# Kernel optimization log

Measured on AMD Instinct MI355X. Metric: run time of the kernel, lower is better.

Reference implementation:

```python
import jax, jax.numpy as jnp
import numpy as np

H = 4096      # hidden_size
HQ = 32       # num_attention_heads
HKV = 8       # num_key_value_heads
D = 128       # head_dim
I = 14336     # intermediate_size
T = 2048      # number of tokens (prefill)
THETA = 500000.0
EPS = 1e-5


def setup_inputs() -> dict:
    key = jax.random.key(0)
    ks = jax.random.split(key, 9)
    s = 0.02
    return {
        "hidden_states": jax.random.normal(ks[0], (T, H), jnp.float32),
        "position_ids": jnp.arange(T, dtype=jnp.int32),
        "w_q": jax.random.normal(ks[1], (H, H), jnp.float32) * s,
        "w_k": jax.random.normal(ks[2], (HKV * D, H), jnp.float32) * s,
        "w_v": jax.random.normal(ks[3], (HKV * D, H), jnp.float32) * s,
        "w_o": jax.random.normal(ks[4], (H, H), jnp.float32) * s,
        "w_gate": jax.random.normal(ks[5], (I, H), jnp.float32) * s,
        "w_up": jax.random.normal(ks[6], (I, H), jnp.float32) * s,
        "w_down": jax.random.normal(ks[7], (H, I), jnp.float32) * s,
        "rms1_w": jnp.ones((H,), jnp.float32),
        "rms2_w": jnp.ones((H,), jnp.float32),
    }


def _rmsnorm(x, w, eps=EPS):
    var = jnp.mean(jnp.square(x), axis=-1, keepdims=True)
    return x * jax.lax.rsqrt(var + eps) * w


def _rope(x, pos):
    # x: [T, n_heads, D], non-interleaved (rotate halves)
    inv_freq = 1.0 / (THETA ** (jnp.arange(0, D, 2, dtype=jnp.float32) / D))  # [D/2]
    freqs = pos.astype(jnp.float32)[:, None] * inv_freq[None, :]              # [T, D/2]
    cos = jnp.cos(freqs)[:, None, :]  # [T, 1, D/2]
    sin = jnp.sin(freqs)[:, None, :]
    x1, x2 = x[..., : D // 2], x[..., D // 2:]
    return jnp.concatenate([x1 * cos - x2 * sin, x2 * cos + x1 * sin], axis=-1)


def reference(hidden_states, position_ids, w_q, w_k, w_v, w_o,
              w_gate, w_up, w_down, rms1_w, rms2_w):
    x = hidden_states  # [T, H]
    # ---- attention block ----
    h = _rmsnorm(x, rms1_w)
    q = (h @ w_q.T).reshape(T, HQ, D)
    k = (h @ w_k.T).reshape(T, HKV, D)
    v = (h @ w_v.T).reshape(T, HKV, D)
    q = _rope(q, position_ids)
    k = _rope(k, position_ids)
    # GQA: expand kv heads to query heads
    group = HQ // HKV
    k = jnp.repeat(k, group, axis=1)  # [T, HQ, D]
    v = jnp.repeat(v, group, axis=1)
    scale = 1.0 / jnp.sqrt(jnp.float32(D))
    scores = jnp.einsum("qhd,khd->hqk", q, k) * scale  # [HQ, T, T]
    causal = jnp.tril(jnp.ones((T, T), dtype=bool))
    scores = jnp.where(causal[None, :, :], scores, jnp.finfo(scores.dtype).min)
    probs = jax.nn.softmax(scores, axis=-1)
    attn = jnp.einsum("hqk,khd->qhd", probs, v).reshape(T, H)
    x = x + attn @ w_o.T
    # ---- MLP block (SwiGLU) ----
    h = _rmsnorm(x, rms2_w)
    gate = jax.nn.silu(h @ w_gate.T)
    up = h @ w_up.T
    x = x + (gate * up) @ w_down.T
    return x
```

## Files before the change

kernel.cpp:

```cpp
#include <hip/hip_runtime.h>
#include <hip/hip_bf16.h>

#define T_ 2048
#define H_ 4096
#define HQ_ 32
#define HKV_ 8
#define D_ 128
#define I_ 14336

typedef __attribute__((ext_vector_type(8))) short bf16x8;
typedef __attribute__((ext_vector_type(4))) float f32x4;

__device__ __forceinline__ float bf2f(short s) {
    return __uint_as_float(((unsigned int)(unsigned short)s) << 16);
}
__device__ __forceinline__ short f2bf(float f) {
    __hip_bfloat16 h = __float2bfloat16(f);
    unsigned short u;
    __builtin_memcpy(&u, &h, 2);
    return (short)u;
}

__global__ __launch_bounds__(256) void rmsnorm_kernel(
    const float* __restrict__ x, const float* __restrict__ w,
    __hip_bfloat16* __restrict__ out)
{
    int t = blockIdx.x, tid = threadIdx.x;
    const float4* xp = (const float4*)(x + (size_t)t * H_);
    float4 v[4];
    float ss = 0.f;
#pragma unroll
    for (int i = 0; i < 4; ++i) {
        v[i] = xp[i * 256 + tid];
        ss += v[i].x * v[i].x + v[i].y * v[i].y + v[i].z * v[i].z + v[i].w * v[i].w;
    }
#pragma unroll
    for (int off = 32; off; off >>= 1) ss += __shfl_xor(ss, off, 64);
    __shared__ float red[4];
    int wave = tid >> 6, lane = tid & 63;
    if (lane == 0) red[wave] = ss;
    __syncthreads();
    float scale = rsqrtf((red[0] + red[1] + red[2] + red[3]) * (1.0f / H_) + 1e-5f);
    const float4* wp = (const float4*)w;
    uint2* op = (uint2*)(out + (size_t)t * H_);
#pragma unroll
    for (int i = 0; i < 4; ++i) {
        float4 wv = wp[i * 256 + tid];
        union { unsigned short u[4]; uint2 d; } o;
        o.u[0] = (unsigned short)f2bf(v[i].x * scale * wv.x);
        o.u[1] = (unsigned short)f2bf(v[i].y * scale * wv.y);
        o.u[2] = (unsigned short)f2bf(v[i].z * scale * wv.z);
        o.u[3] = (unsigned short)f2bf(v[i].w * scale * wv.w);
        op[i * 256 + tid] = o.d;
    }
}

template <int RESADD>
__global__ __launch_bounds__(256) void gemm_kernel(
    const __hip_bfloat16* __restrict__ A, const float* __restrict__ B,
    void* __restrict__ Cout, const float* __restrict__ res,
    int M, int N, int K)
{
    constexpr int BM = 128, BN = 128, BK = 32, LDA = 40;
    __shared__ __align__(16) __hip_bfloat16 As[BM * LDA];
    __shared__ __align__(16) __hip_bfloat16 Bs[BN * LDA];
    int tid = threadIdx.x;
    int wave = tid >> 6, lane = tid & 63, ln = lane & 15, quad = lane >> 4;
    int wr = wave >> 1, wc = wave & 1;
    int m0 = blockIdx.x * BM, n0 = blockIdx.y * BN;
    int srow = tid >> 1, shalf = tid & 1;

    f32x4 acc[4][4] = {};

    const uint4*  ag = (const uint4*)(A + (size_t)(m0 + srow) * K + shalf * 16);
    const float4* bg = (const float4*)(B + (size_t)(n0 + srow) * K + shalf * 16);

    for (int k0 = 0; k0 < K; k0 += BK) {
        uint4 a0 = ag[0], a1 = ag[1];
        ag += 4;
        float4 b0 = bg[0], b1 = bg[1], b2 = bg[2], b3 = bg[3];
        bg += 8;
        __syncthreads();
        *(uint4*)&As[srow * LDA + shalf * 16]     = a0;
        *(uint4*)&As[srow * LDA + shalf * 16 + 8] = a1;
        union { uint4 q[2]; unsigned short u[16]; } bb;
        float bf[16] = { b0.x, b0.y, b0.z, b0.w, b1.x, b1.y, b1.z, b1.w,
                         b2.x, b2.y, b2.z, b2.w, b3.x, b3.y, b3.z, b3.w };
#pragma unroll
        for (int j = 0; j < 16; ++j) bb.u[j] = (unsigned short)f2bf(bf[j]);
        *(uint4*)&Bs[srow * LDA + shalf * 16]     = bb.q[0];
        *(uint4*)&Bs[srow * LDA + shalf * 16 + 8] = bb.q[1];
        __syncthreads();

        bf16x8 af[4], bfr[4];
#pragma unroll
        for (int i = 0; i < 4; ++i)
            af[i] = *(const bf16x8*)&As[(wr * 64 + i * 16 + ln) * LDA + quad * 8];
#pragma unroll
        for (int j = 0; j < 4; ++j)
            bfr[j] = *(const bf16x8*)&Bs[(wc * 64 + j * 16 + ln) * LDA + quad * 8];
#pragma unroll
        for (int i = 0; i < 4; ++i)
#pragma unroll
            for (int j = 0; j < 4; ++j)
                acc[i][j] = __builtin_amdgcn_mfma_f32_16x16x32_bf16(af[i], bfr[j], acc[i][j], 0, 0, 0);
    }

#pragma unroll
    for (int i = 0; i < 4; ++i)
#pragma unroll
        for (int j = 0; j < 4; ++j)
#pragma unroll
            for (int r = 0; r < 4; ++r) {
                int row = m0 + wr * 64 + i * 16 + quad * 4 + r;
                int col = n0 + wc * 64 + j * 16 + ln;
                if (RESADD) {
                    ((float*)Cout)[(size_t)row * N + col] =
                        acc[i][j][r] + res[(size_t)row * N + col];
                } else {
                    ((__hip_bfloat16*)Cout)[(size_t)row * N + col] =
                        __float2bfloat16(acc[i][j][r]);
                }
            }
}

__global__ __launch_bounds__(64) void rope_kernel(
    __hip_bfloat16* __restrict__ q, __hip_bfloat16* __restrict__ k,
    const int* __restrict__ pos)
{
    int t = blockIdx.x, h = blockIdx.y, i = threadIdx.x;
    float p = (float)pos[t];
    float inv = powf(500000.0f, -(float)i * (1.0f / 64.0f));
    float s, c;
    sincosf(p * inv, &s, &c);
    __hip_bfloat16* base = (h < HQ_) ? (q + ((size_t)t * HQ_ + h) * D_)
                                     : (k + ((size_t)t * HKV_ + (h - HQ_)) * D_);
    float x1 = bf2f(*(short*)&base[i]);
    float x2 = bf2f(*(short*)&base[i + 64]);
    base[i]      = __float2bfloat16(x1 * c - x2 * s);
    base[i + 64] = __float2bfloat16(x2 * c + x1 * s);
}

__global__ __launch_bounds__(256) void attn_kernel(
    const __hip_bfloat16* __restrict__ Q,
    const __hip_bfloat16* __restrict__ K,
    const __hip_bfloat16* __restrict__ V,
    __hip_bfloat16* __restrict__ O)
{
    constexpr float scale = 0.08838834764831845f;
    int qtile = blockIdx.x, hq = blockIdx.y, hkv = hq >> 2;
    int tid = threadIdx.x;
    int wave = tid >> 6, lane = tid & 63, ln = lane & 15, quad = lane >> 4;
    int q0 = qtile * 64;

    __shared__ __align__(16) __hip_bfloat16 Kt[32 * 136];
    __shared__ __align__(16) __hip_bfloat16 Vt[128 * 40];
    __shared__ __align__(16) __hip_bfloat16 Pb[4][16 * 40];

    bf16x8 qf[4];
    {
        const __hip_bfloat16* qp = Q + ((size_t)(q0 + wave * 16 + ln) * HQ_ + hq) * D_;
#pragma unroll
        for (int kc = 0; kc < 4; ++kc)
            qf[kc] = *(const bf16x8*)(qp + kc * 32 + quad * 8);
    }

    f32x4 o_acc[8] = {};
    float m_run[4] = { -3e38f, -3e38f, -3e38f, -3e38f };
    float l_run[4] = { 0.f, 0.f, 0.f, 0.f };

    int nkt = (q0 + 64) / 32;
    int sr = tid >> 3, sseg = tid & 7;
    for (int kt = 0; kt < nkt; ++kt) {
        int k0 = kt * 32;
        {
            const __hip_bfloat16* kp = K + ((size_t)(k0 + sr) * HKV_ + hkv) * D_ + sseg * 16;
            uint4 k01 = ((const uint4*)kp)[0], k23 = ((const uint4*)kp)[1];
            *(uint4*)&Kt[sr * 136 + sseg * 16]     = k01;
            *(uint4*)&Kt[sr * 136 + sseg * 16 + 8] = k23;
            const __hip_bfloat16* vp = V + ((size_t)(k0 + sr) * HKV_ + hkv) * D_ + sseg * 16;
            union { uint4 q[2]; __hip_bfloat16 h[16]; } vv;
            vv.q[0] = ((const uint4*)vp)[0];
            vv.q[1] = ((const uint4*)vp)[1];
#pragma unroll
            for (int i = 0; i < 16; ++i) Vt[(sseg * 16 + i) * 40 + sr] = vv.h[i];
        }
        __syncthreads();

        f32x4 s_acc[2] = {};
#pragma unroll
        for (int ct = 0; ct < 2; ++ct)
#pragma unroll
            for (int kc = 0; kc < 4; ++kc) {
                bf16x8 kf = *(const bf16x8*)&Kt[(ct * 16 + ln) * 136 + kc * 32 + quad * 8];
                s_acc[ct] = __builtin_amdgcn_mfma_f32_16x16x32_bf16(qf[kc], kf, s_acc[ct], 0, 0, 0);
            }

        float pv[2][4], tmax[4];
#pragma unroll
        for (int r = 0; r < 4; ++r) {
            int qr = q0 + wave * 16 + quad * 4 + r;
            float s0 = s_acc[0][r] * scale;
            float s1 = s_acc[1][r] * scale;
            if (k0 + ln > qr) s0 = -1e30f;
            if (k0 + 16 + ln > qr) s1 = -1e30f;
            pv[0][r] = s0; pv[1][r] = s1;
            tmax[r] = fmaxf(s0, s1);
        }
#pragma unroll
        for (int off = 1; off < 16; off <<= 1)
#pragma unroll
            for (int r = 0; r < 4; ++r)
                tmax[r] = fmaxf(tmax[r], __shfl_xor(tmax[r], off, 64));

        float alpha[4], tsum[4];
#pragma unroll
        for (int r = 0; r < 4; ++r) {
            float mn = fmaxf(m_run[r], tmax[r]);
            alpha[r] = __expf(m_run[r] - mn);
            m_run[r] = mn;
            float p0 = __expf(pv[0][r] - mn);
            float p1 = __expf(pv[1][r] - mn);
            pv[0][r] = p0; pv[1][r] = p1;
            tsum[r] = p0 + p1;
        }
#pragma unroll
        for (int off = 1; off < 16; off <<= 1)
#pragma unroll
            for (int r = 0; r < 4; ++r)
                tsum[r] += __shfl_xor(tsum[r], off, 64);
#pragma unroll
        for (int r = 0; r < 4; ++r) l_run[r] = l_run[r] * alpha[r] + tsum[r];
#pragma unroll
        for (int nt = 0; nt < 8; ++nt)
#pragma unroll
            for (int r = 0; r < 4; ++r) o_acc[nt][r] *= alpha[r];

#pragma unroll
        for (int r = 0; r < 4; ++r) {
            Pb[wave][(quad * 4 + r) * 40 + ln]      = __float2bfloat16(pv[0][r]);
            Pb[wave][(quad * 4 + r) * 40 + 16 + ln] = __float2bfloat16(pv[1][r]);
        }
        asm volatile("s_waitcnt lgkmcnt(0)" ::: "memory");

        bf16x8 pf = *(const bf16x8*)&Pb[wave][ln * 40 + quad * 8];
#pragma unroll
        for (int nt = 0; nt < 8; ++nt) {
            bf16x8 vf = *(const bf16x8*)&Vt[(nt * 16 + ln) * 40 + quad * 8];
            o_acc[nt] = __builtin_amdgcn_mfma_f32_16x16x32_bf16(pf, vf, o_acc[nt], 0, 0, 0);
        }
        __syncthreads();
    }

    float inv_l[4];
#pragma unroll
    for (int r = 0; r < 4; ++r) inv_l[r] = 1.0f / l_run[r];
#pragma unroll
    for (int nt = 0; nt < 8; ++nt)
#pragma unroll
        for (int r = 0; r < 4; ++r) {
            int qr = q0 + wave * 16 + quad * 4 + r;
            O[(size_t)qr * H_ + hq * D_ + nt * 16 + ln] =
                __float2bfloat16(o_acc[nt][r] * inv_l[r]);
        }
}

__global__ __launch_bounds__(256) void silu_mul_kernel(
    __hip_bfloat16* __restrict__ gate, const __hip_bfloat16* __restrict__ up)
{
    size_t idx = (size_t)blockIdx.x * 256 + threadIdx.x;
    bf16x8 g = ((const bf16x8*)gate)[idx];
    bf16x8 u = ((const bf16x8*)up)[idx];
    bf16x8 o;
#pragma unroll
    for (int j = 0; j < 8; ++j) {
        float gf = bf2f(g[j]);
        float uf = bf2f(u[j]);
        float r = gf / (1.0f + __expf(-gf)) * uf;
        o[j] = f2bf(r);
    }
    ((bf16x8*)gate)[idx] = o;
}

extern "C" void kernel_launch(void* const* d_in, const int* in_sizes, int n_in,
                              void* d_out, int out_size, void* d_ws, size_t ws_size,
                              hipStream_t stream) {
    const float* x_in   = (const float*)d_in[0];
    const int*   pos    = (const int*)d_in[1];
    const float* w_q    = (const float*)d_in[2];
    const float* w_k    = (const float*)d_in[3];
    const float* w_v    = (const float*)d_in[4];
    const float* w_o    = (const float*)d_in[5];
    const float* w_gate = (const float*)d_in[6];
    const float* w_up   = (const float*)d_in[7];
    const float* w_down = (const float*)d_in[8];
    const float* rms1   = (const float*)d_in[9];
    const float* rms2   = (const float*)d_in[10];
    float* out = (float*)d_out;

    char* ws = (char*)d_ws;
    size_t off = 0;
    auto alloc = [&](size_t bytes) {
        void* p = ws + off;
        off += (bytes + 255) & ~(size_t)255;
        return p;
    };
    __hip_bfloat16* hb   = (__hip_bfloat16*)alloc((size_t)T_ * H_ * 2);
    __hip_bfloat16* qb   = (__hip_bfloat16*)alloc((size_t)T_ * HQ_ * D_ * 2);
    __hip_bfloat16* kb   = (__hip_bfloat16*)alloc((size_t)T_ * HKV_ * D_ * 2);
    __hip_bfloat16* vb   = (__hip_bfloat16*)alloc((size_t)T_ * HKV_ * D_ * 2);
    float*          x1   = (float*)alloc((size_t)T_ * H_ * 4);
    __hip_bfloat16* gate = (__hip_bfloat16*)alloc((size_t)T_ * I_ * 2);
    __hip_bfloat16* up   = (__hip_bfloat16*)alloc((size_t)T_ * I_ * 2);

    rmsnorm_kernel<<<T_, 256, 0, stream>>>(x_in, rms1, hb);
    gemm_kernel<0><<<dim3(16, 32), 256, 0, stream>>>(hb, w_q, qb, nullptr, T_, H_, H_);
    gemm_kernel<0><<<dim3(16, 8), 256, 0, stream>>>(hb, w_k, kb, nullptr, T_, HKV_ * D_, H_);
    gemm_kernel<0><<<dim3(16, 8), 256, 0, stream>>>(hb, w_v, vb, nullptr, T_, HKV_ * D_, H_);
    rope_kernel<<<dim3(T_, HQ_ + HKV_), 64, 0, stream>>>(qb, kb, pos);
    attn_kernel<<<dim3(32, 32), 256, 0, stream>>>(qb, kb, vb, hb);
    gemm_kernel<1><<<dim3(16, 32), 256, 0, stream>>>(hb, w_o, x1, x_in, T_, H_, H_);
    rmsnorm_kernel<<<T_, 256, 0, stream>>>(x1, rms2, qb);
    gemm_kernel<0><<<dim3(16, 112), 256, 0, stream>>>(qb, w_gate, gate, nullptr, T_, I_, H_);
    gemm_kernel<0><<<dim3(16, 112), 256, 0, stream>>>(qb, w_up, up, nullptr, T_, I_, H_);
    silu_mul_kernel<<<(T_ * I_ / 8) / 256, 256, 0, stream>>>(gate, up);
    gemm_kernel<1><<<dim3(16, 32), 256, 0, stream>>>(gate, w_down, out, x1, T_, H_, I_);
}
```

Measured before the change: 2.996 ms.

## Pre-convert weights to bf16 and stage GEMM tiles via direct global-to-LDS loads

Adds a pass that converts every fp32 weight matrix to bf16 in workspace on each call. The GEMM then reads bf16 weights through global_load_lds 16-byte direct-to-LDS copies instead of loading fp32, converting in registers and storing to padded LDS. Workgroup IDs are also remapped so consecutive tiles land on the same XCD for better L2 reuse. Costs include an extra read and write of all weights per call and unpadded LDS rows, which may cause bank conflicts on the fragment reads.

```diff
diff --git a/kernel.cpp b/kernel.cpp
--- a/kernel.cpp
+++ b/kernel.cpp
@@ -19,6 +19,30 @@
     unsigned short u;
     __builtin_memcpy(&u, &h, 2);
     return (short)u;
+}
+
+__device__ __forceinline__ void gload_lds16(const void* g, void* l) {
+    __builtin_amdgcn_global_load_lds(
+        (const __attribute__((address_space(1))) void*)g,
+        (__attribute__((address_space(3))) void*)l, 16, 0, 0);
+}
+
+__global__ __launch_bounds__(256) void w2bf_kernel(
+    const float* __restrict__ src, __hip_bfloat16* __restrict__ dst)
+{
+    size_t idx = ((size_t)blockIdx.x * 256 + threadIdx.x) * 8;
+    float4 a = *(const float4*)(src + idx);
+    float4 b = *(const float4*)(src + idx + 4);
+    union { unsigned short u[8]; uint4 q; } o;
+    o.u[0] = (unsigned short)f2bf(a.x);
+    o.u[1] = (unsigned short)f2bf(a.y);
+    o.u[2] = (unsigned short)f2bf(a.z);
+    o.u[3] = (unsigned short)f2bf(a.w);
+    o.u[4] = (unsigned short)f2bf(b.x);
+    o.u[5] = (unsigned short)f2bf(b.y);
+    o.u[6] = (unsigned short)f2bf(b.z);
+    o.u[7] = (unsigned short)f2bf(b.w);
+    *(uint4*)(dst + idx) = o.q;
 }
 
 __global__ __launch_bounds__(256) void rmsnorm_kernel(
@@ -57,48 +81,53 @@
 
 template <int RESADD>
 __global__ __launch_bounds__(256) void gemm_kernel(
-    const __hip_bfloat16* __restrict__ A, const float* __restrict__ B,
+    const __hip_bfloat16* __restrict__ A, const __hip_bfloat16* __restrict__ B,
     void* __restrict__ Cout, const float* __restrict__ res,
     int M, int N, int K)
 {
-    constexpr int BM = 128, BN = 128, BK = 32, LDA = 40;
-    __shared__ __align__(16) __hip_bfloat16 As[BM * LDA];
-    __shared__ __align__(16) __hip_bfloat16 Bs[BN * LDA];
+    constexpr int BM = 128, BN = 128, BK = 32;
+    __shared__ __align__(16) __hip_bfloat16 As[BM * BK];
+    __shared__ __align__(16) __hip_bfloat16 Bs[BN * BK];
     int tid = threadIdx.x;
     int wave = tid >> 6, lane = tid & 63, ln = lane & 15, quad = lane >> 4;
     int wr = wave >> 1, wc = wave & 1;
-    int m0 = blockIdx.x * BM, n0 = blockIdx.y * BN;
-    int srow = tid >> 1, shalf = tid & 1;
+
+    int nwg = gridDim.x * gridDim.y;
+    int orig = blockIdx.y * gridDim.x + blockIdx.x;
+    int xcd = orig & 7, loc = orig >> 3;
+    int qq = nwg >> 3, rr = nwg & 7;
+    int swz = (xcd < rr ? xcd * (qq + 1) : rr * (qq + 1) + (xcd - rr) * qq) + loc;
+    int m0 = (swz % gridDim.x) * BM;
+    int n0 = (swz / gridDim.x) * BN;
+
+    int row = tid >> 2, slot = tid & 3;
+    const __hip_bfloat16* ga0 = A + (size_t)(m0 + row) * K + slot * 8;
+    const __hip_bfloat16* ga1 = A + (size_t)(m0 + 64 + row) * K + slot * 8;
+    const __hip_bfloat16* gb0 = B + (size_t)(n0 + row) * K + slot * 8;
+    const __hip_bfloat16* gb1 = B + (size_t)(n0 + 64 + row) * K + slot * 8;
+    __hip_bfloat16* la0 = As + tid * 8;
+    __hip_bfloat16* la1 = As + 2048 + tid * 8;
+    __hip_bfloat16* lb0 = Bs + tid * 8;
+    __hip_bfloat16* lb1 = Bs + 2048 + tid * 8;
 
     f32x4 acc[4][4] = {};
 
-    const uint4*  ag = (const uint4*)(A + (size_t)(m0 + srow) * K + shalf * 16);
-    const float4* bg = (const float4*)(B + (size_t)(n0 + srow) * K + shalf * 16);
-
     for (int k0 = 0; k0 < K; k0 += BK) {
-        uint4 a0 = ag[0], a1 = ag[1];
-        ag += 4;
-        float4 b0 = bg[0], b1 = bg[1], b2 = bg[2], b3 = bg[3];
-        bg += 8;
         __syncthreads();
-        *(uint4*)&As[srow * LDA + shalf * 16]     = a0;
-        *(uint4*)&As[srow * LDA + shalf * 16 + 8] = a1;
-        union { uint4 q[2]; unsigned short u[16]; } bb;
-        float bf[16] = { b0.x, b0.y, b0.z, b0.w, b1.x, b1.y, b1.z, b1.w,
-                         b2.x, b2.y, b2.z, b2.w, b3.x, b3.y, b3.z, b3.w };
-#pragma unroll
-        for (int j = 0; j < 16; ++j) bb.u[j] = (unsigned short)f2bf(bf[j]);
-        *(uint4*)&Bs[srow * LDA + shalf * 16]     = bb.q[0];
-        *(uint4*)&Bs[srow * LDA + shalf * 16 + 8] = bb.q[1];
+        gload_lds16(ga0, la0);
+        gload_lds16(ga1, la1);
+        gload_lds16(gb0, lb0);
+        gload_lds16(gb1, lb1);
+        ga0 += BK; ga1 += BK; gb0 += BK; gb1 += BK;
         __syncthreads();
 
         bf16x8 af[4], bfr[4];
 #pragma unroll
         for (int i = 0; i < 4; ++i)
-            af[i] = *(const bf16x8*)&As[(wr * 64 + i * 16 + ln) * LDA + quad * 8];
+            af[i] = *(const bf16x8*)&As[(wr * 64 + i * 16 + ln) * BK + quad * 8];
 #pragma unroll
         for (int j = 0; j < 4; ++j)
-            bfr[j] = *(const bf16x8*)&Bs[(wc * 64 + j * 16 + ln) * LDA + quad * 8];
+            bfr[j] = *(const bf16x8*)&Bs[(wc * 64 + j * 16 + ln) * BK + quad * 8];
 #pragma unroll
         for (int i = 0; i < 4; ++i)
 #pragma unroll
@@ -112,13 +141,13 @@
         for (int j = 0; j < 4; ++j)
 #pragma unroll
             for (int r = 0; r < 4; ++r) {
-                int row = m0 + wr * 64 + i * 16 + quad * 4 + r;
-                int col = n0 + wc * 64 + j * 16 + ln;
+                int row_ = m0 + wr * 64 + i * 16 + quad * 4 + r;
+                int col_ = n0 + wc * 64 + j * 16 + ln;
                 if (RESADD) {
-                    ((float*)Cout)[(size_t)row * N + col] =
-                        acc[i][j][r] + res[(size_t)row * N + col];
+                    ((float*)Cout)[(size_t)row_ * N + col_] =
+                        acc[i][j][r] + res[(size_t)row_ * N + col_];
                 } else {
-                    ((__hip_bfloat16*)Cout)[(size_t)row * N + col] =
+                    ((__hip_bfloat16*)Cout)[(size_t)row_ * N + col_] =
                         __float2bfloat16(acc[i][j][r]);
                 }
             }
@@ -312,17 +341,35 @@
     float*          x1   = (float*)alloc((size_t)T_ * H_ * 4);
     __hip_bfloat16* gate = (__hip_bfloat16*)alloc((size_t)T_ * I_ * 2);
     __hip_bfloat16* up   = (__hip_bfloat16*)alloc((size_t)T_ * I_ * 2);
+    __hip_bfloat16* wqb  = (__hip_bfloat16*)alloc((size_t)H_ * H_ * 2);
+    __hip_bfloat16* wkb  = (__hip_bfloat16*)alloc((size_t)HKV_ * D_ * H_ * 2);
+    __hip_bfloat16* wvb  = (__hip_bfloat16*)alloc((size_t)HKV_ * D_ * H_ * 2);
+    __hip_bfloat16* wob  = (__hip_bfloat16*)alloc((size_t)H_ * H_ * 2);
+    __hip_bfloat16* wgb  = (__hip_bfloat16*)alloc((size_t)I_ * H_ * 2);
+    __hip_bfloat16* wub  = (__hip_bfloat16*)alloc((size_t)I_ * H_ * 2);
+    __hip_bfloat16* wdb  = (__hip_bfloat16*)alloc((size_t)H_ * I_ * 2);
+
+    auto cvt = [&](const float* s, __hip_bfloat16* d, size_t n) {
+        w2bf_kernel<<<(unsigned)(n / 2048), 256, 0, stream>>>(s, d);
+    };
+    cvt(w_q,    wqb, (size_t)H_ * H_);
+    cvt(w_k,    wkb, (size_t)HKV_ * D_ * H_);
+    cvt(w_v,    wvb, (size_t)HKV_ * D_ * H_);
+    cvt(w_o,    wob, (size_t)H_ * H_);
+    cvt(w_gate, wgb, (size_t)I_ * H_);
+    cvt(w_up,   wub, (size_t)I_ * H_);
+    cvt(w_down, wdb, (size_t)H_ * I_);
 
     rmsnorm_kernel<<<T_, 256, 0, stream>>>(x_in, rms1, hb);
-    gemm_kernel<0><<<dim3(16, 32), 256, 0, stream>>>(hb, w_q, qb, nullptr, T_, H_, H_);
-    gemm_kernel<0><<<dim3(16, 8), 256, 0, stream>>>(hb, w_k, kb, nullptr, T_, HKV_ * D_, H_);
-    gemm_kernel<0><<<dim3(16, 8), 256, 0, stream>>>(hb, w_v, vb, nullptr, T_, HKV_ * D_, H_);
+    gemm_kernel<0><<<dim3(16, 32), 256, 0, stream>>>(hb, wqb, qb, nullptr, T_, H_, H_);
+    gemm_kernel<0><<<dim3(16, 8), 256, 0, stream>>>(hb, wkb, kb, nullptr, T_, HKV_ * D_, H_);
+    gemm_kernel<0><<<dim3(16, 8), 256, 0, stream>>>(hb, wvb, vb, nullptr, T_, HKV_ * D_, H_);
     rope_kernel<<<dim3(T_, HQ_ + HKV_), 64, 0, stream>>>(qb, kb, pos);
     attn_kernel<<<dim3(32, 32), 256, 0, stream>>>(qb, kb, vb, hb);
-    gemm_kernel<1><<<dim3(16, 32), 256, 0, stream>>>(hb, w_o, x1, x_in, T_, H_, H_);
+    gemm_kernel<1><<<dim3(16, 32), 256, 0, stream>>>(hb, wob, x1, x_in, T_, H_, H_);
     rmsnorm_kernel<<<T_, 256, 0, stream>>>(x1, rms2, qb);
-    gemm_kernel<0><<<dim3(16, 112), 256, 0, stream>>>(qb, w_gate, gate, nullptr, T_, I_, H_);
-    gemm_kernel<0><<<dim3(16, 112), 256, 0, stream>>>(qb, w_up, up, nullptr, T_, I_, H_);
+    gemm_kernel<0><<<dim3(16, 112), 256, 0, stream>>>(qb, wgb, gate, nullptr, T_, I_, H_);
+    gemm_kernel<0><<<dim3(16, 112), 256, 0, stream>>>(qb, wub, up, nullptr, T_, I_, H_);
     silu_mul_kernel<<<(T_ * I_ / 8) / 256, 256, 0, stream>>>(gate, up);
-    gemm_kernel<1><<<dim3(16, 32), 256, 0, stream>>>(gate, w_down, out, x1, T_, H_, I_);
-}
+    gemm_kernel<1><<<dim3(16, 32), 256, 0, stream>>>(gate, wdb, out, x1, T_, H_, I_);
+}
```

Measured after the change: 2.722 ms. 9.1% less time.
